# Kernel tuning notes

Measured on AMD Instinct MI355X. Metric: run time of the kernel, lower is better.

## Reference

```python
import jax, jax.numpy as jnp
import numpy as np

V, E, D = 50000, 800000, 128
EH, NH = 128, 128  # edge_hidden, node_hidden


def setup_inputs() -> dict:
    key = jax.random.key(0)
    ks = jax.random.split(key, 12)
    h = jax.random.normal(ks[0], (V, D), dtype=jnp.float32)
    edge_index = jax.random.randint(ks[1], (2, E), 0, V, dtype=jnp.int64)
    s = 0.02
    # edge MLP: Linear(2D->EH), Linear(EH->EH), Linear(EH->NH)
    W1 = jax.random.normal(ks[2], (2 * D, EH), dtype=jnp.float32) * s
    b1 = jnp.zeros((EH,), dtype=jnp.float32)
    W2 = jax.random.normal(ks[3], (EH, EH), dtype=jnp.float32) * s
    b2 = jnp.zeros((EH,), dtype=jnp.float32)
    W3 = jax.random.normal(ks[4], (EH, NH), dtype=jnp.float32) * s
    b3 = jnp.zeros((NH,), dtype=jnp.float32)
    # node MLP: Linear(D+NH->NH), Linear(NH->NH)
    Wn1 = jax.random.normal(ks[5], (D + NH, NH), dtype=jnp.float32) * s
    bn1 = jnp.zeros((NH,), dtype=jnp.float32)
    Wn2 = jax.random.normal(ks[6], (NH, NH), dtype=jnp.float32) * s
    bn2 = jnp.zeros((NH,), dtype=jnp.float32)
    return {"h": h, "edge_index": edge_index, "W1": W1, "b1": b1, "W2": W2,
            "b2": b2, "W3": W3, "b3": b3, "Wn1": Wn1, "bn1": bn1,
            "Wn2": Wn2, "bn2": bn2}


def reference(h, edge_index, W1, b1, W2, b2, W3, b3, Wn1, bn1, Wn2, bn2):
    src, dst = edge_index[0], edge_index[1]
    # gather node pairs -> edge features (E, 2D)
    edge_feat = jnp.concatenate([h[src], h[dst]], axis=-1)
    # 3-layer edge MLP
    m = jax.nn.relu(edge_feat @ W1 + b1)
    m = jax.nn.relu(m @ W2 + b2)
    messages = m @ W3 + b3                       # (E, NH)
    # scatter-add into destination nodes
    agg = jax.ops.segment_sum(messages, dst, num_segments=h.shape[0])  # (V, NH)
    # node MLP on [h, agg]
    x = jnp.concatenate([h, agg], axis=-1)       # (V, D+NH)
    out = jax.nn.relu(x @ Wn1 + bn1) @ Wn2 + bn2  # (V, NH)
    return out
```

## Files before the change

### kernel.cpp

```cpp
#include <hip/hip_runtime.h>

#define NV 50000
#define NE 800000
#define CVT_N 1600000
#define TR_N  81920
#define W3N_N 16384
#define B3N_N 128
#define NB1 49
#define NB_PERM 3125
#define NB_H1 196
#define SCAP 12

typedef _Float16 f16x8 __attribute__((ext_vector_type(8)));
typedef _Float16 f16x4 __attribute__((ext_vector_type(4)));
typedef float    f32x4 __attribute__((ext_vector_type(4)));

static __device__ __forceinline__ f32x4 mfma16(f16x8 a, f16x8 b, f32x4 c) {
  return __builtin_amdgcn_mfma_f32_16x16x32_f16(a, b, c, 0, 0, 0);
}

__global__ void prep_kernel(const float* __restrict__ h, _Float16* __restrict__ hf,
    const float* __restrict__ W1, const float* __restrict__ W2, const float* __restrict__ W3,
    const float* __restrict__ Wn1, const float* __restrict__ Wn2, const float* __restrict__ b3,
    _Float16* __restrict__ w1st, _Float16* __restrict__ w1dt, _Float16* __restrict__ w2t,
    _Float16* __restrict__ wn1c, _Float16* __restrict__ wn2t, float* __restrict__ b3n,
    const int* __restrict__ ei, int* __restrict__ counts)
{
  int i = blockIdx.x * blockDim.x + threadIdx.x;
  if (i < CVT_N) {
    f32x4 v = reinterpret_cast<const f32x4*>(h)[i];
    f16x4 o;
    o[0] = (_Float16)v[0]; o[1] = (_Float16)v[1]; o[2] = (_Float16)v[2]; o[3] = (_Float16)v[3];
    reinterpret_cast<f16x4*>(hf)[i] = o;
    return;
  }
  i -= CVT_N;
  if (i < TR_N) {
    int seg = i >> 14;
    int j = i & 16383;
    int f = j >> 7, k = j & 127;
    switch (seg) {
      case 0: w1st[j] = (_Float16)W1[k * 128 + f]; break;
      case 1: w1dt[j] = (_Float16)W1[(k + 128) * 128 + f]; break;
      case 2: w2t[j]  = (_Float16)W2[k * 128 + f]; break;
      case 3: wn1c[f * 256 + k] = (_Float16)Wn1[k * 128 + f]; break;
      case 4: wn2t[j] = (_Float16)Wn2[k * 128 + f]; break;
    }
    return;
  }
  i -= TR_N;
  if (i < W3N_N) {
    int f = i >> 7, ii = i & 127;
    float a = 0.f;
    for (int j = 0; j < 128; j++) a += W3[ii * 128 + j] * Wn1[(128 + j) * 128 + f];
    wn1c[f * 256 + 128 + ii] = (_Float16)a;
    return;
  }
  i -= W3N_N;
  if (i < B3N_N) {
    float a = 0.f;
    for (int j = 0; j < 128; j++) a += b3[j] * Wn1[(128 + j) * 128 + i];
    b3n[i] = a;
    return;
  }
  i -= B3N_N;
  if (i < NE) atomicAdd(&counts[ei[NE + i]], 1);
}

__global__ __launch_bounds__(1024)
void bsum_kernel(const int* __restrict__ counts, int* __restrict__ bsum) {
  __shared__ int red[1024];
  const int t = threadIdx.x;
  int i = blockIdx.x * 1024 + t;
  red[t] = (i < NV) ? counts[i] : 0;
  __syncthreads();
  for (int off = 512; off > 0; off >>= 1) {
    if (t < off) red[t] += red[t + off];
    __syncthreads();
  }
  if (t == 0) bsum[blockIdx.x] = red[0];
}

__global__ __launch_bounds__(1024)
void offs_kernel(const int* __restrict__ counts, const int* __restrict__ bsum,
                 int* __restrict__ offsets, int* __restrict__ cursor) {
  __shared__ int s[1024];
  __shared__ int sbase;
  const int t = threadIdx.x;
  int i = blockIdx.x * 1024 + t;
  int v = (i < NV) ? counts[i] : 0;
  s[t] = v;
  if (t < 64) {
    int x = (t < blockIdx.x) ? bsum[t] : 0;
    for (int off = 1; off < 64; off <<= 1) x += __shfl_xor(x, off);
    if (t == 0) sbase = x;
  }
  __syncthreads();
  for (int off = 1; off < 1024; off <<= 1) {
    int x = (t >= off) ? s[t - off] : 0;
    __syncthreads();
    s[t] += x;
    __syncthreads();
  }
  if (i < NV) {
    int excl = sbase + s[t] - v;
    offsets[i] = excl;
    cursor[i] = excl;
    if (i == NV - 1) offsets[NV] = sbase + s[t];
  }
}

static __device__ __forceinline__ void gemm128_rows(
    const _Float16* __restrict__ hf, const int* nid, const _Float16* __restrict__ At,
    const float* __restrict__ bias, _Float16* __restrict__ Out,
    int nbase, int l15, int quad)
{
  f32x4 acc[8][4];
#pragma unroll
  for (int mt = 0; mt < 8; mt++)
#pragma unroll
    for (int nt = 0; nt < 4; nt++)
      acc[mt][nt] = (f32x4){0.f, 0.f, 0.f, 0.f};

  f16x8 Bc[4], Bn[4];
#pragma unroll
  for (int nt = 0; nt < 4; nt++)
    Bc[nt] = *reinterpret_cast<const f16x8*>(hf + (long long)nid[nt] * 128 + quad * 8);
#pragma unroll
  for (int s = 0; s < 4; s++) {
    if (s < 3) {
#pragma unroll
      for (int nt = 0; nt < 4; nt++)
        Bn[nt] = *reinterpret_cast<const f16x8*>(hf + (long long)nid[nt] * 128 + (s + 1) * 32 + quad * 8);
    }
    const int k = s * 32 + quad * 8;
#pragma unroll
    for (int mt = 0; mt < 8; mt++) {
      f16x8 A = *reinterpret_cast<const f16x8*>(At + (mt * 16 + l15) * 128 + k);
#pragma unroll
      for (int nt = 0; nt < 4; nt++)
        acc[mt][nt] = mfma16(A, Bc[nt], acc[mt][nt]);
    }
#pragma unroll
    for (int nt = 0; nt < 4; nt++) Bc[nt] = Bn[nt];
  }
#pragma unroll
  for (int mt = 0; mt < 8; mt++) {
    f32x4 bb = bias ? *reinterpret_cast<const f32x4*>(bias + mt * 16 + quad * 4)
                    : (f32x4){0.f, 0.f, 0.f, 0.f};
#pragma unroll
    for (int nt = 0; nt < 4; nt++) {
      int n = nbase + nt * 16 + l15;
      if (n < NV) {
        f16x4 o;
#pragma unroll
        for (int r = 0; r < 4; r++) o[r] = (_Float16)(acc[mt][nt][r] + bb[r]);
        *reinterpret_cast<f16x4*>(Out + (long long)n * 128 + mt * 16 + quad * 4) = o;
      }
    }
  }
}

__global__ __launch_bounds__(256, 2)
void h1p_kernel(const _Float16* __restrict__ hf, const float* __restrict__ b1,
                const _Float16* __restrict__ w1st, const _Float16* __restrict__ w1dt,
                _Float16* __restrict__ H1s, _Float16* __restrict__ H1d,
                const int* __restrict__ ei, int* __restrict__ cursor,
                int2* __restrict__ pairs)
{
  int bx = blockIdx.x;
  if (bx < NB_PERM) {
    int e = bx * 256 + threadIdx.x;
    int s = ei[e], d = ei[NE + e];
    int pos = atomicAdd(&cursor[d], 1);
    pairs[pos] = make_int2(s, d);
    return;
  }
  bx -= NB_PERM;
  const int by = bx & 1;
  const int bxx = bx >> 1;
  const int t = threadIdx.x;
  const int lane = t & 63, wave = t >> 6;
  const int quad = lane >> 4, l15 = lane & 15;
  const int nbase = bxx * 256 + wave * 64;
  int nid[4];
#pragma unroll
  for (int nt = 0; nt < 4; nt++) {
    int n = nbase + nt * 16 + l15;
    nid[nt] = n < NV ? n : NV - 1;
  }
  if (by == 0) gemm128_rows(hf, nid, w1st, nullptr, H1s, nbase, l15, quad);
  else         gemm128_rows(hf, nid, w1dt, b1,      H1d, nbase, l15, quad);
}

__global__ __launch_bounds__(128, 2)
void edge_kernel(const _Float16* __restrict__ H1s, const _Float16* __restrict__ H1d,
                 const int2* __restrict__ pairs,
                 const _Float16* __restrict__ w2t, const float* __restrict__ b2,
                 float* __restrict__ agg2)
{
  __shared__ __align__(16) _Float16 M2t[128 * 128];
  __shared__ __align__(16) _Float16 H1ds[2 * SCAP][136];
  __shared__ int segdst2[2][64];
  __shared__ __align__(8) unsigned char sseg8[128];
  __shared__ unsigned long long wmask[2];
  __shared__ int snbr[4];

  const int t = threadIdx.x;
  const int lane = t & 63, wave = t >> 6;
  const int quad = lane >> 4, l15 = lane & 15;
  const int ebase = blockIdx.x * 128;
  const int wbase = wave * 64;

  const int2 prt = pairs[ebase + t];
  const int dprev = (t > 0) ? pairs[ebase + t - 1].y : -1;
  if (t == 0)   snbr[0] = (ebase > 0) ? pairs[ebase - 1].y : -1;
  if (t == 1)   snbr[1] = (ebase + 128 < NE) ? pairs[ebase + 128].y : -1;
  if (t == 0)   snbr[2] = prt.y;
  if (t == 127) snbr[3] = prt.y;

  const bool flag = (t > 0) && (prt.y != dprev);
  const unsigned long long bm = __ballot(flag);
  if (lane == 0) wmask[wave] = bm;
  const int pre = (int)__popcll(bm & ((1ull << lane) - 1ull)) + (flag ? 1 : 0);
  sseg8[t] = (unsigned char)pre;
  if (flag || lane == 0) segdst2[wave][pre] = prt.y;

  int esrc[4], edst[4], lsid[4];
#pragma unroll
  for (int et = 0; et < 4; et++) {
    int2 q = pairs[ebase + wbase + et * 16 + l15];
    esrc[et] = q.x; edst[et] = q.y;
    lsid[et] = __shfl(pre, et * 16 + l15);
  }

  f16x8 h1r[4][4];
#pragma unroll
  for (int et = 0; et < 4; et++)
#pragma unroll
    for (int s = 0; s < 4; s++)
      h1r[et][s] = *reinterpret_cast<const f16x8*>(H1s + (long long)esrc[et] * 128 + s * 32 + quad * 8);

  if ((flag || lane == 0) && pre < SCAP) {
    const _Float16* src = H1d + (long long)prt.y * 128;
    _Float16* drow = &H1ds[wave * SCAP + pre][0];
#pragma unroll
    for (int b = 0; b < 2; b++) {
      f16x8 tmp[8];
#pragma unroll
      for (int c = 0; c < 8; c++)
        tmp[c] = *reinterpret_cast<const f16x8*>(src + (b * 8 + c) * 8);
#pragma unroll
      for (int c = 0; c < 8; c++)
        *reinterpret_cast<f16x8*>(drow + (b * 8 + c) * 8) = tmp[c];
    }
  }
  asm volatile("s_waitcnt lgkmcnt(0)" ::: "memory");
  __builtin_amdgcn_sched_barrier(0);

  f16x8 m1f[4][4];
#pragma unroll
  for (int et = 0; et < 4; et++) {
    const int ls = lsid[et];
    const bool useL = ls < SCAP;
    const _Float16* lrow = &H1ds[wave * SCAP + (useL ? ls : 0)][0];
    const _Float16* grow = H1d + (long long)edst[et] * 128;
#pragma unroll
    for (int s = 0; s < 4; s++) {
      f16x8 b;
      if (useL) b = *reinterpret_cast<const f16x8*>(lrow + s * 32 + quad * 8);
      else      b = *reinterpret_cast<const f16x8*>(grow + s * 32 + quad * 8);
      f16x8 o = h1r[et][s] + b;
#pragma unroll
      for (int j = 0; j < 8; j++) o[j] = o[j] > (_Float16)0 ? o[j] : (_Float16)0;
      m1f[et][s] = o;
    }
  }

  float b2v[8];
#pragma unroll
  for (int ft = 0; ft < 8; ft++) b2v[ft] = b2[ft * 16 + l15];

  f32x4 acc[4][8];
#pragma unroll
  for (int et = 0; et < 4; et++)
#pragma unroll
    for (int ft = 0; ft < 8; ft++)
      acc[et][ft] = (f32x4){0.f, 0.f, 0.f, 0.f};

#pragma unroll
  for (int s = 0; s < 4; s++) {
    const int k = s * 32 + quad * 8;
#pragma unroll
    for (int ft = 0; ft < 8; ft++) {
      f16x8 B = *reinterpret_cast<const f16x8*>(w2t + (ft * 16 + l15) * 128 + k);
#pragma unroll
      for (int et = 0; et < 4; et++)
        acc[et][ft] = mfma16(m1f[et][s], B, acc[et][ft]);
    }
  }
#pragma unroll
  for (int et = 0; et < 4; et++) {
    const int g = wave * 16 + et * 4 + quad;
#pragma unroll
    for (int ft = 0; ft < 8; ft++) {
      const int f = ft * 16 + l15;
      f16x4 o;
#pragma unroll
      for (int r = 0; r < 4; r++) {
        float x = acc[et][ft][r] + b2v[ft];
        o[r] = (_Float16)(x > 0.f ? x : 0.f);
      }
      *reinterpret_cast<f16x4*>(&M2t[f * 128 + ((g ^ (l15 << 1)) * 4)]) = o;
    }
  }
  __syncthreads();

  const int c0 = (int)__popcll(wmask[0]);
  const int c1 = (int)__popcll(wmask[1]);
  const int nseg = c0 + c1 + 1;
  const int nmt = (nseg + 15) >> 4;
  const bool openL = (snbr[2] == snbr[0]);
  const bool openR = (snbr[3] == snbr[1]);

  f16x8 Bf[4][4];
#pragma unroll
  for (int fl = 0; fl < 4; fl++) {
    const int f = (wave * 4 + fl) * 16 + l15;
#pragma unroll
    for (int s = 0; s < 4; s++) {
      const int g0 = s * 8 + quad * 2;
      Bf[fl][s] = *reinterpret_cast<const f16x8*>(&M2t[f * 128 + ((g0 ^ (l15 << 1)) * 4)]);
    }
  }
  unsigned long long segb[4];
#pragma unroll
  for (int s = 0; s < 4; s++)
    segb[s] = *reinterpret_cast<const unsigned long long*>(&sseg8[s * 32 + quad * 8]);

  for (int mt = 0; mt < nmt; mt++) {
    const int myseg = mt * 16 + l15;
    f32x4 racc[4];
#pragma unroll
    for (int fl = 0; fl < 4; fl++) racc[fl] = (f32x4){0.f, 0.f, 0.f, 0.f};
#pragma unroll
    for (int s = 0; s < 4; s++) {
      const int target = myseg - ((s >= 2) ? c0 : 0);
      f16x8 S;
#pragma unroll
      for (int j = 0; j < 8; j++)
        S[j] = ((int)((segb[s] >> (8 * j)) & 255ull) == target) ? (_Float16)1 : (_Float16)0;
#pragma unroll
      for (int fl = 0; fl < 4; fl++)
        racc[fl] = mfma16(S, Bf[fl][s], racc[fl]);
    }
#pragma unroll
    for (int fl = 0; fl < 4; fl++) {
      const int f = (wave * 4 + fl) * 16 + l15;
#pragma unroll
      for (int r = 0; r < 4; r++) {
        const int sg = mt * 16 + quad * 4 + r;
        if (sg < nseg) {
          float v = racc[fl][r];
          const int dst = (sg <= c0) ? segdst2[0][sg] : segdst2[1][sg - c0];
          float* p = agg2 + (long long)dst * 128 + f;
          const bool at = (sg == 0 && openL) || (sg == nseg - 1 && openR);
          if (at) unsafeAtomicAdd(p, v); else *p = v;
        }
      }
    }
  }
}

__global__ __launch_bounds__(256, 2)
void node_kernel(const _Float16* __restrict__ hf, const float* __restrict__ agg2,
                 const int* __restrict__ offsets,
                 const _Float16* __restrict__ wn1c, const float* __restrict__ bn1,
                 const float* __restrict__ b3n,
                 const _Float16* __restrict__ wn2t, const float* __restrict__ bn2,
                 float* __restrict__ out)
{
  __shared__ __align__(16) _Float16 M[256 * 128];
  const int t = threadIdx.x;
  const int lane = t & 63, wave = t >> 6;
  const int quad = lane >> 4, l15 = lane & 15;
  const int wbase = wave * 64;
  const int nbase = blockIdx.x * 256 + wbase;

  int nid[4]; float fcnt[4];
#pragma unroll
  for (int nt = 0; nt < 4; nt++) {
    int n = nbase + nt * 16 + l15;
    nid[nt] = n < NV ? n : NV - 1;
    fcnt[nt] = (n < NV) ? (float)(offsets[n + 1] - offsets[n]) : 0.f;
  }

  f32x4 acc[8][4];
#pragma unroll
  for (int mt = 0; mt < 8; mt++)
#pragma unroll
    for (int nt = 0; nt < 4; nt++)
      acc[mt][nt] = (f32x4){0.f, 0.f, 0.f, 0.f};

  f16x8 Bc[4], Bn[4];
#pragma unroll
  for (int nt = 0; nt < 4; nt++)
    Bc[nt] = *reinterpret_cast<const f16x8*>(hf + (long long)nid[nt] * 128 + quad * 8);
#pragma unroll
  for (int s = 0; s < 8; s++) {
    if (s < 7) {
      const int sn = s + 1;
      if (sn < 4) {
#pragma unroll
        for (int nt = 0; nt < 4; nt++)
          Bn[nt] = *reinterpret_cast<const f16x8*>(hf + (long long)nid[nt] * 128 + sn * 32 + quad * 8);
      } else {
#pragma unroll
        for (int nt = 0; nt < 4; nt++) {
          const float* ap = agg2 + (long long)nid[nt] * 128 + (sn - 4) * 32 + quad * 8;
          f32x4 a0 = *reinterpret_cast<const f32x4*>(ap);
          f32x4 a1 = *reinterpret_cast<const f32x4*>(ap + 4);
          f16x8 bb;
#pragma unroll
          for (int j = 0; j < 4; j++) { bb[j] = (_Float16)a0[j]; bb[4 + j] = (_Float16)a1[j]; }
          Bn[nt] = bb;
        }
      }
    }
    const int k = s * 32 + quad * 8;
#pragma unroll
    for (int mt = 0; mt < 8; mt++) {
      f16x8 A = *reinterpret_cast<const f16x8*>(wn1c + (mt * 16 + l15) * 256 + k);
#pragma unroll
      for (int nt = 0; nt < 4; nt++)
        acc[mt][nt] = mfma16(A, Bc[nt], acc[mt][nt]);
    }
#pragma unroll
    for (int nt = 0; nt < 4; nt++) Bc[nt] = Bn[nt];
  }
#pragma unroll
  for (int mt = 0; mt < 8; mt++) {
    f32x4 bb  = *reinterpret_cast<const f32x4*>(bn1 + mt * 16 + quad * 4);
    f32x4 b3c = *reinterpret_cast<const f32x4*>(b3n + mt * 16 + quad * 4);
    const int cbase = 2 * mt + (quad >> 1);
#pragma unroll
    for (int nt = 0; nt < 4; nt++) {
      int row = wbase + nt * 16 + l15;
      int c = cbase ^ (row & 15);
      f16x4 o;
#pragma unroll
      for (int r = 0; r < 4; r++) {
        float x = acc[mt][nt][r] + bb[r] + fcnt[nt] * b3c[r];
        o[r] = (_Float16)(x > 0.f ? x : 0.f);
      }
      *reinterpret_cast<f16x4*>(&M[row * 128 + c * 8 + (quad & 1) * 4]) = o;
      acc[mt][nt] = (f32x4){0.f, 0.f, 0.f, 0.f};
    }
  }

#pragma unroll
  for (int s = 0; s < 4; s++) {
    f16x8 B[4];
#pragma unroll
    for (int nt = 0; nt < 4; nt++) {
      int row = wbase + nt * 16 + l15;
      B[nt] = *reinterpret_cast<const f16x8*>(&M[row * 128 + (((4 * s + quad) ^ (row & 15)) * 8)]);
    }
    const int k = s * 32 + quad * 8;
#pragma unroll
    for (int mt = 0; mt < 8; mt++) {
      f16x8 A = *reinterpret_cast<const f16x8*>(wn2t + (mt * 16 + l15) * 128 + k);
#pragma unroll
      for (int nt = 0; nt < 4; nt++)
        acc[mt][nt] = mfma16(A, B[nt], acc[mt][nt]);
    }
  }
#pragma unroll
  for (int mt = 0; mt < 8; mt++) {
    f32x4 bias = *reinterpret_cast<const f32x4*>(bn2 + mt * 16 + quad * 4);
#pragma unroll
    for (int nt = 0; nt < 4; nt++) {
      int n = nbase + nt * 16 + l15;
      if (n < NV) {
        f32x4 v;
#pragma unroll
        for (int r = 0; r < 4; r++) v[r] = acc[mt][nt][r] + bias[r];
        *reinterpret_cast<f32x4*>(out + (long long)n * 128 + mt * 16 + quad * 4) = v;
      }
    }
  }
}

static inline size_t align16(size_t x) { return (x + 15) & ~(size_t)15; }

extern "C" void kernel_launch(void* const* d_in, const int* in_sizes, int n_in,
                              void* d_out, int out_size, void* d_ws, size_t ws_size,
                              hipStream_t stream)
{
  const float* h   = (const float*)d_in[0];
  const int*   ei  = (const int*)d_in[1];
  const float* W1  = (const float*)d_in[2];
  const float* b1  = (const float*)d_in[3];
  const float* W2  = (const float*)d_in[4];
  const float* b2  = (const float*)d_in[5];
  const float* W3  = (const float*)d_in[6];
  const float* b3  = (const float*)d_in[7];
  const float* Wn1 = (const float*)d_in[8];
  const float* bn1 = (const float*)d_in[9];
  const float* Wn2 = (const float*)d_in[10];
  const float* bn2 = (const float*)d_in[11];
  float* out = (float*)d_out;

  char* p = (char*)d_ws;
  _Float16* hf   = (_Float16*)p; p += align16((size_t)NV * 128 * 2);
  _Float16* H1s  = (_Float16*)p; p += align16((size_t)NV * 128 * 2);
  _Float16* H1d  = (_Float16*)p; p += align16((size_t)NV * 128 * 2);
  _Float16* w1st = (_Float16*)p; p += align16(128 * 128 * 2);
  _Float16* w1dt = (_Float16*)p; p += align16(128 * 128 * 2);
  _Float16* w2t  = (_Float16*)p; p += align16(128 * 128 * 2);
  _Float16* wn1c = (_Float16*)p; p += align16(128 * 256 * 2);
  _Float16* wn2t = (_Float16*)p; p += align16(128 * 128 * 2);
  float*  b3n  = (float*)p;  p += align16(128 * 4);
  int* counts  = (int*)p; p += align16((size_t)NV * 4);
  int* offsets = (int*)p; p += align16((size_t)(NV + 1) * 4);
  int* cursor  = (int*)p; p += align16((size_t)NV * 4);
  int* bsum    = (int*)p; p += align16((size_t)(NB1 + 1) * 4);
  int2* pairs  = (int2*)p; p += align16((size_t)NE * 8);
  float* agg2  = (float*)p; p += align16((size_t)NV * 128 * 4);

  hipMemsetAsync(counts, 0, (size_t)NV * 4, stream);
  hipMemsetAsync(agg2, 0, (size_t)NV * 128 * 4, stream);
  {
    int total = CVT_N + TR_N + W3N_N + B3N_N + NE;
    prep_kernel<<<(total + 255) / 256, 256, 0, stream>>>(
        h, hf, W1, W2, W3, Wn1, Wn2, b3,
        w1st, w1dt, w2t, wn1c, wn2t, b3n, ei, counts);
  }
  bsum_kernel<<<NB1, 1024, 0, stream>>>(counts, bsum);
  offs_kernel<<<NB1, 1024, 0, stream>>>(counts, bsum, offsets, cursor);
  h1p_kernel<<<NB_PERM + 2 * NB_H1, 256, 0, stream>>>(hf, b1, w1st, w1dt, H1s, H1d,
                                                      ei, cursor, pairs);
  edge_kernel<<<NE / 128, 128, 0, stream>>>(H1s, H1d, pairs, w2t, b2, agg2);
  node_kernel<<<(NV + 255) / 256, 256, 0, stream>>>(hf, agg2, offsets, wn1c, bn1, b3n,
                                                    wn2t, bn2, out);
}
```

Before: 379.0 us.

## Fuse agg2 zeroing into h1p kernel and drop LDS staging of H1d rows

```diff
diff --git a/kernel.cpp b/kernel.cpp
--- a/kernel.cpp
+++ b/kernel.cpp
@@ -7,9 +7,9 @@
 #define W3N_N 16384
 #define B3N_N 128
 #define NB1 49
+#define NB_ZERO 6250
 #define NB_PERM 3125
 #define NB_H1 196
-#define SCAP 12
 
 typedef _Float16 f16x8 __attribute__((ext_vector_type(8)));
 typedef _Float16 f16x4 __attribute__((ext_vector_type(4)));
@@ -166,9 +166,14 @@
                 const _Float16* __restrict__ w1st, const _Float16* __restrict__ w1dt,
                 _Float16* __restrict__ H1s, _Float16* __restrict__ H1d,
                 const int* __restrict__ ei, int* __restrict__ cursor,
-                int2* __restrict__ pairs)
+                int2* __restrict__ pairs, float* __restrict__ agg2)
 {
   int bx = blockIdx.x;
+  if (bx < NB_ZERO) {
+    reinterpret_cast<f32x4*>(agg2)[bx * 256 + threadIdx.x] = (f32x4){0.f, 0.f, 0.f, 0.f};
+    return;
+  }
+  bx -= NB_ZERO;
   if (bx < NB_PERM) {
     int e = bx * 256 + threadIdx.x;
     int s = ei[e], d = ei[NE + e];
@@ -200,7 +205,6 @@
                  float* __restrict__ agg2)
 {
   __shared__ __align__(16) _Float16 M2t[128 * 128];
-  __shared__ __align__(16) _Float16 H1ds[2 * SCAP][136];
   __shared__ int segdst2[2][64];
   __shared__ __align__(8) unsigned char sseg8[128];
   __shared__ unsigned long long wmask[2];
@@ -226,51 +230,21 @@
   sseg8[t] = (unsigned char)pre;
   if (flag || lane == 0) segdst2[wave][pre] = prt.y;
 
-  int esrc[4], edst[4], lsid[4];
+  int esrc[4], edst[4];
 #pragma unroll
   for (int et = 0; et < 4; et++) {
     int2 q = pairs[ebase + wbase + et * 16 + l15];
     esrc[et] = q.x; edst[et] = q.y;
-    lsid[et] = __shfl(pre, et * 16 + l15);
-  }
-
-  f16x8 h1r[4][4];
-#pragma unroll
-  for (int et = 0; et < 4; et++)
-#pragma unroll
-    for (int s = 0; s < 4; s++)
-      h1r[et][s] = *reinterpret_cast<const f16x8*>(H1s + (long long)esrc[et] * 128 + s * 32 + quad * 8);
-
-  if ((flag || lane == 0) && pre < SCAP) {
-    const _Float16* src = H1d + (long long)prt.y * 128;
-    _Float16* drow = &H1ds[wave * SCAP + pre][0];
-#pragma unroll
-    for (int b = 0; b < 2; b++) {
-      f16x8 tmp[8];
-#pragma unroll
-      for (int c = 0; c < 8; c++)
-        tmp[c] = *reinterpret_cast<const f16x8*>(src + (b * 8 + c) * 8);
-#pragma unroll
-      for (int c = 0; c < 8; c++)
-        *reinterpret_cast<f16x8*>(drow + (b * 8 + c) * 8) = tmp[c];
-    }
-  }
-  asm volatile("s_waitcnt lgkmcnt(0)" ::: "memory");
-  __builtin_amdgcn_sched_barrier(0);
+  }
 
   f16x8 m1f[4][4];
 #pragma unroll
   for (int et = 0; et < 4; et++) {
-    const int ls = lsid[et];
-    const bool useL = ls < SCAP;
-    const _Float16* lrow = &H1ds[wave * SCAP + (useL ? ls : 0)][0];
-    const _Float16* grow = H1d + (long long)edst[et] * 128;
 #pragma unroll
     for (int s = 0; s < 4; s++) {
-      f16x8 b;
-      if (useL) b = *reinterpret_cast<const f16x8*>(lrow + s * 32 + quad * 8);
-      else      b = *reinterpret_cast<const f16x8*>(grow + s * 32 + quad * 8);
-      f16x8 o = h1r[et][s] + b;
+      f16x8 a = *reinterpret_cast<const f16x8*>(H1s + (long long)esrc[et] * 128 + s * 32 + quad * 8);
+      f16x8 b = *reinterpret_cast<const f16x8*>(H1d + (long long)edst[et] * 128 + s * 32 + quad * 8);
+      f16x8 o = a + b;
 #pragma unroll
       for (int j = 0; j < 8; j++) o[j] = o[j] > (_Float16)0 ? o[j] : (_Float16)0;
       m1f[et][s] = o;
@@ -529,7 +503,6 @@
   float* agg2  = (float*)p; p += align16((size_t)NV * 128 * 4);
 
   hipMemsetAsync(counts, 0, (size_t)NV * 4, stream);
-  hipMemsetAsync(agg2, 0, (size_t)NV * 128 * 4, stream);
   {
     int total = CVT_N + TR_N + W3N_N + B3N_N + NE;
     prep_kernel<<<(total + 255) / 256, 256, 0, stream>>>(
@@ -538,8 +511,8 @@
   }
   bsum_kernel<<<NB1, 1024, 0, stream>>>(counts, bsum);
   offs_kernel<<<NB1, 1024, 0, stream>>>(counts, bsum, offsets, cursor);
-  h1p_kernel<<<NB_PERM + 2 * NB_H1, 256, 0, stream>>>(hf, b1, w1st, w1dt, H1s, H1d,
-                                                      ei, cursor, pairs);
+  h1p_kernel<<<NB_ZERO + NB_PERM + 2 * NB_H1, 256, 0, stream>>>(
+      hf, b1, w1st, w1dt, H1s, H1d, ei, cursor, pairs, agg2);
   edge_kernel<<<NE / 128, 128, 0, stream>>>(H1s, H1d, pairs, w2t, b2, agg2);
   node_kernel<<<(NV + 255) / 256, 256, 0, stream>>>(hf, agg2, offsets, wn1c, bn1, b3n,
                                                     wn2t, bn2, out);
```

New measurement: 354.1 us. -6.6%, faster.
